# Optimization experiments

Measured on AMD Instinct MI355X. Metric: run time of the kernel, lower is better.

The kernel has to match this reference:

```python
import jax, jax.numpy as jnp
import numpy as np

K_NEIGHBORS = 16
NUM_PATCHES = 32
W_NORMAL = 1.0
W_SURFVAR = 1.0


def _knn_centered(points, k):
    """points: [B, N, 3] -> k nearest neighbors re-centered at each point, [B, N, k, 3].
    Distances are computed on stop_gradient(points) to match torch's .detach()."""
    pd = jax.lax.stop_gradient(points)
    # squared pairwise distances [B, N, N] (sqrt is monotone -> topk order identical)
    d2 = jnp.sum((pd[:, :, None, :] - pd[:, None, :, :]) ** 2, axis=-1)
    _, idx = jax.lax.top_k(-d2, k)  # smallest-k indices, [B, N, k]
    knn = jax.vmap(lambda pts, id_: pts[id_])(points, idx)  # [B, N, k, 3]
    return knn - points[:, :, None, :]


def _eig_props(knn):
    """knn: [B, N, k, 3] -> (normal [B,N,3] = eigvec of smallest eigval, eigvals [B,N,3] ascending)."""
    cov = jnp.einsum('bnki,bnkj->bnij', knn, knn)  # [B, N, 3, 3]
    w, v = jnp.linalg.eigh(cov)  # ascending eigenvalues, matches torch.symeig
    return v[..., :, 0], w


def setup_inputs() -> dict:
    key = jax.random.key(0)
    pointCloud = jax.random.normal(key, (4, 8192, 3), dtype=jnp.float32)
    return {"pointCloud": pointCloud}


def reference(pointCloud):
    B, N, _ = pointCloud.shape
    pp = N // NUM_PATCHES

    # global kNN / normals / surface variance
    knn_g = _knn_centered(pointCloud, K_NEIGHBORS)
    nrm_g, w_g = _eig_props(knn_g)

    # patchwise: each patch is an independent small point cloud -> fold patches into batch
    patch_pts = pointCloud.reshape(B * NUM_PATCHES, pp, 3)
    knn_p = _knn_centered(patch_pts, K_NEIGHBORS)
    nrm_p, w_p = _eig_props(knn_p)
    nrm_p = nrm_p.reshape(B, N, 3)

    # normal loss (abs variant, sign-ambiguity-free)
    loss_n = jnp.mean(jnp.linalg.norm(jnp.abs(nrm_p) - jnp.abs(nrm_g), axis=2)) * W_NORMAL

    # surface variance loss: lambda_min / sum(lambda)
    sv_g = w_g[..., 0] / jnp.sum(w_g, axis=-1)            # [B, N]
    sv_p = (w_p[..., 0] / jnp.sum(w_p, axis=-1)).reshape(B, N)
    loss_sv = jnp.mean((sv_p - sv_g) ** 2) * W_SURFVAR

    return jnp.stack([loss_n, loss_sv])  # [2] (original returns list of two [1] tensors)
```

## Files before the change

kernel.cpp:

```cpp
#include <hip/hip_runtime.h>
#include <math.h>

#define KNN 16
#define NPTS 8192
#define PTCH 256
#define NPATCH 32
#define NBATCH 4
#define SSTRIDE 130
#define LAMBDA_T 48.0f

#define GTAB 512
#define RMAX 6.5f
#define GH (RMAX / (float)GTAB)

#define NC 16
#define NCELLS (NC * NC * NC)
#define GMIN -4.2f
#define ICS 1.9047619f

__device__ __forceinline__ float lam_f(float r, float s)
{
    const float C     = 0.063493636f;
    const float SQ2PI = 2.5066283f;
    const float IS2   = 0.70710678f;
    float a = fabsf(r - s), b = r + s;
    float amr = a - r;
    float coefA = amr * amr + 2.f - s * s;
    float I = 2.f * __expf(-0.5f * b * b) - coefA * __expf(-0.5f * a * a)
            + r * SQ2PI * (erff(b * IS2) - erff(a * IS2));
    float M = C * (3.14159265f / r) * I;
    if (s > r) {
        float u = s - r;
        M += 12.566371f * C * (1.2533141f * erff(u * IS2) - u * __expf(-0.5f * u * u));
    }
    return (float)NPTS * M;
}

__device__ __forceinline__ void jrot(double& app, double& aqq, double& apq,
                                     double& arp, double& arq,
                                     double& vp0, double& vq0,
                                     double& vp1, double& vq1,
                                     double& vp2, double& vq2)
{
    double g = apq;
    if (g == 0.0) return;
    double theta = (aqq - app) / (2.0 * g);
    double at = fabs(theta);
    double t = (at > 1.0e154) ? (0.5 / theta)
                              : (copysign(1.0, theta) / (at + sqrt(theta * theta + 1.0)));
    double c = 1.0 / sqrt(t * t + 1.0);
    double s = t * c;
    double tau = s / (1.0 + c);
    app -= t * g;
    aqq += t * g;
    apq = 0.0;
    double rp = arp, rq = arq;
    arp = rp - s * (rq + tau * rp);
    arq = rq + s * (rp - tau * rq);
    double p0 = vp0, q0 = vq0;
    vp0 = p0 - s * (q0 + tau * p0); vq0 = q0 + s * (p0 - tau * q0);
    double p1 = vp1, q1 = vq1;
    vp1 = p1 - s * (q1 + tau * p1); vq1 = q1 + s * (p1 - tau * q1);
    double p2 = vp2, q2 = vq2;
    vp2 = p2 - s * (q2 + tau * p2); vq2 = q2 + s * (p2 - tau * q2);
}

__device__ __forceinline__ void eig3(double a00, double a11, double a22,
                                     double a01, double a02, double a12,
                                     double& nx, double& ny, double& nz,
                                     double& lmin, double& lsum)
{
    double v00 = 1, v01 = 0, v02 = 0;
    double v10 = 0, v11 = 1, v12 = 0;
    double v20 = 0, v21 = 0, v22 = 1;
    double scale = fabs(a00) + fabs(a11) + fabs(a22) + fabs(a01) + fabs(a02) + fabs(a12);
    if (scale > 0.0) {
        for (int sweep = 0; sweep < 6; ++sweep) {
            double off = fabs(a01) + fabs(a02) + fabs(a12);
            if (off <= scale * 1e-15) break;
            jrot(a00, a11, a01, a02, a12, v00, v01, v10, v11, v20, v21);
            jrot(a00, a22, a02, a01, a12, v00, v02, v10, v12, v20, v22);
            jrot(a11, a22, a12, a01, a02, v01, v02, v11, v12, v21, v22);
        }
    }
    lsum = a00 + a11 + a22;
    lmin = a00; nx = v00; ny = v10; nz = v20;
    if (a11 < lmin) { lmin = a11; nx = v01; ny = v11; nz = v21; }
    if (a22 < lmin) { lmin = a22; nx = v02; ny = v12; nz = v22; }
}

__device__ __forceinline__ unsigned mkkey(float d2, unsigned idx) {
    return (__float_as_uint(d2) & 0xFFFFE000u) | idx;
}

__device__ __forceinline__ void insert16(unsigned key, unsigned* L)
{
    L[KNN - 1] = key;
    #pragma unroll
    for (int m = KNN - 1; m >= 1; --m) {
        unsigned a = L[m - 1], b = L[m];
        L[m - 1] = min(a, b);
        L[m]     = max(a, b);
    }
}

__device__ __forceinline__ void merge4(unsigned* L, int lane)
{
    #pragma unroll
    for (int step = 1; step <= 2; step <<= 1) {
        unsigned tmp[KNN];
        #pragma unroll
        for (int m = 0; m < KNN; ++m) tmp[m] = __shfl(L[m], lane ^ step, 64);
        for (int m = 0; m < KNN; ++m) {
            if (tmp[m] >= L[KNN - 1]) break;
            insert16(tmp[m], L);
        }
    }
}

__device__ __forceinline__ unsigned mbcnt64(unsigned long long m) {
    return __builtin_amdgcn_mbcnt_hi((unsigned)(m >> 32),
           __builtin_amdgcn_mbcnt_lo((unsigned)m, 0u));
}

__device__ __forceinline__ int cidx(float v) {
    int i = (int)floorf((v - GMIN) * ICS);
    return min(max(i, 0), NC - 1);
}
__device__ __forceinline__ int cellOf(float x, float y, float z) {
    return (cidx(z) * NC + cidx(y)) * NC + cidx(x);
}

#define BT 1024
__global__ void __launch_bounds__(1024)
build_kernel(const float* __restrict__ pts,
             unsigned* __restrict__ cellStart, float4* __restrict__ sorted,
             float* __restrict__ gtab, unsigned* __restrict__ done)
{
    __shared__ unsigned hist[NCELLS];
    __shared__ unsigned part[BT];
    const int b = blockIdx.x;
    const int t = threadIdx.x;
    if (b == 0 && t == 0) done[0] = 0u;
    for (int i = t; i < NCELLS; i += BT) hist[i] = 0u;
    __syncthreads();
    const float* base = pts + (size_t)b * (NPTS * 3);
    float px[8], py[8], pz[8];
    int pc[8];
    #pragma unroll
    for (int k = 0; k < 8; ++k) {
        int i = k * BT + t;
        px[k] = base[i * 3 + 0];
        py[k] = base[i * 3 + 1];
        pz[k] = base[i * 3 + 2];
        pc[k] = cellOf(px[k], py[k], pz[k]);
        atomicAdd(&hist[pc[k]], 1u);
    }
    __syncthreads();
    unsigned loc[4], s = 0;
    #pragma unroll
    for (int i = 0; i < 4; ++i) { loc[i] = s; s += hist[t * 4 + i]; }
    part[t] = s;
    __syncthreads();
    for (int o = 1; o < BT; o <<= 1) {
        unsigned u = (t >= o) ? part[t - o] : 0u;
        __syncthreads();
        part[t] += u;
        __syncthreads();
    }
    unsigned basex = part[t] - s;
    unsigned* csb = cellStart + b * (NCELLS + 1);
    #pragma unroll
    for (int i = 0; i < 4; ++i) {
        unsigned e = basex + loc[i];
        csb[t * 4 + i] = e;
        hist[t * 4 + i] = e;
    }
    if (t == BT - 1) csb[NCELLS] = basex + s;
    __syncthreads();
    float4* sb = sorted + (size_t)b * NPTS;
    #pragma unroll
    for (int k = 0; k < 8; ++k) {
        int i = k * BT + t;
        unsigned slot = atomicAdd(&hist[pc[k]], 1u);
        float4 v;
        v.x = px[k]; v.y = py[k]; v.z = pz[k]; v.w = __uint_as_float((unsigned)i);
        sb[slot] = v;
    }
    if (b == 0 && t < GTAB) {
        float r = fmaxf((float)(t + 1) * GH, 0.01f);
        float lo = 0.f, hi = 12.f;
        #pragma unroll 1
        for (int it = 0; it < 16; ++it) {
            float mid = 0.5f * (lo + hi);
            if (lam_f(r, mid) < LAMBDA_T) lo = mid; else hi = mid;
        }
        gtab[t] = hi;
    }
}

__global__ void __launch_bounds__(256)
fselect_kernel(const float* __restrict__ pts,
               const unsigned* __restrict__ cellStart,
               const float4* __restrict__ sortedp,
               const float* __restrict__ gtab,
               unsigned* __restrict__ idx16)
{
    __shared__ unsigned survl[4 * SSTRIDE];
    const int t = threadIdx.x;
    const int wv = t >> 6;
    const int lane = t & 63;
    const int wq = __builtin_amdgcn_readfirstlane(blockIdx.x * 4 + wv);
    const int b   = wq >> 13;
    const int pos = wq & (NPTS - 1);
    const float* base = pts + (size_t)b * (NPTS * 3);
    const unsigned* cs = cellStart + b * (NCELLS + 1);
    const float4* sp = sortedp + (size_t)b * NPTS;
    unsigned* sl = survl + wv * SSTRIDE;

    const float4 qc = sp[pos];
    const float qx = qc.x, qy = qc.y, qz = qc.z;
    const int oq = b * NPTS + (int)__float_as_uint(qc.w);

    const float r = sqrtf(qx * qx + qy * qy + qz * qz);
    const int gi = min(GTAB - 1, (int)(r * (1.0f / GH)));
    const float g = gtab[gi];
    const float g2 = g * g;

    int ixlo = cidx(qx - g), ixhi = cidx(qx + g);
    int iylo = cidx(qy - g), iyhi = cidx(qy + g);
    int izlo = cidx(qz - g), izhi = cidx(qz + g);
    int nx = ixhi - ixlo + 1;
    int ny = iyhi - iylo + 1;
    int nyz = ny * (izhi - izlo + 1);
    const int lR  = (nyz >= 8) ? 3 : (nyz >= 4) ? 2 : (nyz >= 2) ? 1 : 0;
    const int R   = 1 << lR;
    const int lsl = 6 - lR;
    const unsigned SL = 64u >> lR;
    const unsigned slot = (unsigned)lane & (SL - 1u);
    unsigned cnt = 0;
    #pragma unroll 1
    for (int r0 = 0; r0 < nyz; r0 += 64) {
        int rr = r0 + lane;
        unsigned pk = 0;
        if (rr < nyz) {
            int iz = izlo + rr / ny;
            int iy = iylo + (rr - (rr / ny) * ny);
            int cb = (iz * NC + iy) * NC + ixlo;
            unsigned sB = cs[cb];
            pk = sB | ((cs[cb + nx] - sB) << 14);
        }
        int rmax = min(nyz - r0, 64);
        int gcount = (rmax + R - 1) >> lR;
        #pragma unroll 1
        for (int gg = 0; gg < gcount; ++gg) {
            unsigned pkm = __shfl(pk, (gg << lR) + (lane >> lsl), 64);
            unsigned sBm = pkm & 0x3FFFu;
            unsigned lm  = pkm >> 14;
            #pragma unroll 1
            for (unsigned st = slot; ; st += 2u * SL) {
                bool in0 = st < lm;
                if (!__any(in0 ? 1 : 0)) break;
                unsigned st1 = st + SL;
                bool in1 = st1 < lm;
                float4 c0 = sp[min(sBm + st,  (unsigned)(NPTS - 1))];
                float4 c1 = sp[min(sBm + st1, (unsigned)(NPTS - 1))];
                float dx0 = qx - c0.x, dy0 = qy - c0.y, dz0 = qz - c0.z;
                float d20 = dx0 * dx0 + dy0 * dy0 + dz0 * dz0;
                float dx1 = qx - c1.x, dy1 = qy - c1.y, dz1 = qz - c1.z;
                float d21 = dx1 * dx1 + dy1 * dy1 + dz1 * dz1;
                bool p0 = in0 && (d20 < g2);
                bool p1 = in1 && (d21 < g2);
                unsigned long long m0 = __ballot(p0);
                unsigned long long m1 = __ballot(p1);
                if (p0) {
                    unsigned sw = min(cnt + mbcnt64(m0), (unsigned)(SSTRIDE - 1));
                    sl[sw] = mkkey(d20, __float_as_uint(c0.w));
                }
                unsigned cn = cnt + (unsigned)__popcll(m0);
                if (p1) {
                    unsigned sw = min(cn + mbcnt64(m1), (unsigned)(SSTRIDE - 1));
                    sl[sw] = mkkey(d21, __float_as_uint(c1.w));
                }
                cnt = cn + (unsigned)__popcll(m1);
            }
        }
    }

    bool valid = (cnt >= KNN) && (cnt <= 128u);
    if (valid) {
        unsigned k0 = (lane < (int)cnt)      ? sl[lane]      : 0xFFFFFFFFu;
        unsigned k1 = (lane + 64 < (int)cnt) ? sl[lane + 64] : 0xFFFFFFFFu;
        unsigned r0 = 0, r1 = 0;
        #pragma unroll 4
        for (unsigned m = 0; m < cnt; ++m) {
            unsigned km = sl[m];
            r0 += (km < k0) ? 1u : 0u;
            r1 += (km < k1) ? 1u : 0u;
        }
        unsigned cand = 0;
        if (lane < (int)cnt && r0 == 15u) cand = k0;
        if (lane + 64 < (int)cnt && r1 == 15u) cand = k1;
        #pragma unroll
        for (int o = 1; o < 64; o <<= 1)
            cand = max(cand, (unsigned)__shfl_xor((int)cand, o, 64));
        float upper = __uint_as_float((cand & 0xFFFFE000u) + 0x2000u);
        valid = (upper < g2 * 0.999f - 1e-5f);
        if (valid) {
            if (lane < (int)cnt && r0 < 16u)
                idx16[(size_t)oq * 32 + r0] = k0 & 0x1FFFu;
            if (lane + 64 < (int)cnt && r1 < 16u)
                idx16[(size_t)oq * 32 + r1] = k1 & 0x1FFFu;
        }
    }
    if (!valid && lane == 0) {
        unsigned gl[KNN];
        #pragma unroll
        for (int m = 0; m < KNN; ++m) gl[m] = 0xFFFFFFFFu;
        #pragma unroll 1
        for (int i = 0; i < NPTS; ++i) {
            float cx = base[i * 3 + 0];
            float cy = base[i * 3 + 1];
            float cz = base[i * 3 + 2];
            float dx = qx - cx, dy = qy - cy, dz = qz - cz;
            float d2 = dx * dx + dy * dy + dz * dz;
            unsigned k = mkkey(d2, (unsigned)i);
            if (k < gl[KNN - 1]) insert16(k, gl);
        }
        unsigned* dst = idx16 + (size_t)oq * 32;
        #pragma unroll
        for (int m = 0; m < KNN; ++m) dst[m] = gl[m] & 0x1FFFu;
    }
}

__global__ void __launch_bounds__(256)
pselect_kernel(const float* __restrict__ pts, unsigned* __restrict__ idx16)
{
    __shared__ float4 pbuf4[PTCH];
    const int t = threadIdx.x;
    const int w = t >> 6;
    const int lane = t & 63;
    const int p = blockIdx.x;
    const int quarter = blockIdx.y;
    const int b = blockIdx.z;
    const float* base = pts + (size_t)b * (NPTS * 3);

    {
        const float* src = base + p * (PTCH * 3);
        float* dst = (float*)pbuf4;
        #pragma unroll
        for (int s = 0; s < 3; ++s) {
            int f = t + s * 256;
            int j = f / 3;
            int c = f - 3 * j;
            dst[j * 4 + c] = src[f];
        }
    }
    __syncthreads();

    const int qq = lane >> 2;
    const int h = lane & 3;
    const int qlocal = quarter * 64 + w * 16 + qq;
    float4 qv = pbuf4[qlocal];
    const float pqx = qv.x, pqy = qv.y, pqz = qv.z;

    unsigned pl[KNN];
    #pragma unroll
    for (int m = 0; m < KNN; ++m) pl[m] = 0xFFFFFFFFu;
    const int j0 = h * 64;
    #pragma unroll 4
    for (int j = j0; j < j0 + 64; ++j) {
        float4 c = pbuf4[j];
        float dx = pqx - c.x, dy = pqy - c.y, dz = pqz - c.z;
        float d2 = dx * dx + dy * dy + dz * dz;
        unsigned k = mkkey(d2, (unsigned)j);
        if (k < pl[KNN - 1]) insert16(k, pl);
    }
    merge4(pl, lane);
    if (h == 0) {
        int qid = b * NPTS + p * PTCH + qlocal;
        unsigned* dst = idx16 + (size_t)qid * 32 + 16;
        #pragma unroll
        for (int m = 0; m < KNN; ++m)
            dst[m] = (unsigned)(p * PTCH) + (pl[m] & 0x1FFFu);
    }
}

__global__ void __launch_bounds__(256)
eig_loss_kernel(const float* __restrict__ pts,
                const unsigned* __restrict__ idx16,
                double* __restrict__ partials,
                unsigned* __restrict__ done,
                float* __restrict__ out)
{
    __shared__ double sln[4], slv[4];
    __shared__ unsigned isLast;
    const int t = threadIdx.x;
    const int e = blockIdx.x * 256 + t;
    const int qid = e >> 1;
    const int b = qid >> 13;
    const int qi = qid & (NPTS - 1);
    const float* base = pts + (size_t)b * (NPTS * 3);

    const double qxd = (double)base[qi * 3 + 0];
    const double qyd = (double)base[qi * 3 + 1];
    const double qzd = (double)base[qi * 3 + 2];

    const unsigned* L = idx16 + (size_t)qid * 32 + (e & 1) * 16;
    double c00 = 0, c11 = 0, c22 = 0, c01 = 0, c02 = 0, c12 = 0;
    #pragma unroll
    for (int m = 0; m < KNN; ++m) {
        int idx = (int)L[m];
        double dx = (double)base[idx * 3 + 0] - qxd;
        double dy = (double)base[idx * 3 + 1] - qyd;
        double dz = (double)base[idx * 3 + 2] - qzd;
        c00 += dx * dx; c11 += dy * dy; c22 += dz * dz;
        c01 += dx * dy; c02 += dx * dz; c12 += dy * dz;
    }
    double nx, ny, nz, lmin, lsum;
    eig3(c00, c11, c22, c01, c02, c12, nx, ny, nz, lmin, lsum);
    double sv = lmin / lsum;

    double onx = __shfl_xor(nx, 1, 64);
    double ony = __shfl_xor(ny, 1, 64);
    double onz = __shfl_xor(nz, 1, 64);
    double osv = __shfl_xor(sv, 1, 64);

    double ln = 0.0, lsv = 0.0;
    if ((e & 1) == 0) {
        double dx = fabs(onx) - fabs(nx);
        double dy = fabs(ony) - fabs(ny);
        double dz = fabs(onz) - fabs(nz);
        ln  = sqrt(dx * dx + dy * dy + dz * dz);
        double ds = osv - sv;
        lsv = ds * ds;
    }
    #pragma unroll
    for (int o = 32; o > 0; o >>= 1) {
        ln  += __shfl_down(ln, o);
        lsv += __shfl_down(lsv, o);
    }
    const int w = t >> 6;
    if ((t & 63) == 0) { sln[w] = ln; slv[w] = lsv; }
    __syncthreads();
    if (t == 0) {
        partials[blockIdx.x * 2 + 0] = sln[0] + sln[1] + sln[2] + sln[3];
        partials[blockIdx.x * 2 + 1] = slv[0] + slv[1] + slv[2] + slv[3];
        __threadfence();
        isLast = (atomicAdd(done, 1u) == (unsigned)(gridDim.x - 1)) ? 1u : 0u;
    }
    __syncthreads();
    if (isLast) {
        double a = partials[t * 2 + 0];
        double c = partials[t * 2 + 1];
        #pragma unroll
        for (int o = 32; o > 0; o >>= 1) {
            a += __shfl_down(a, o);
            c += __shfl_down(c, o);
        }
        if ((t & 63) == 0) { sln[t >> 6] = a; slv[t >> 6] = c; }
        __syncthreads();
        if (t == 0) {
            const double inv = 1.0 / (double)(NBATCH * NPTS);
            out[0] = (float)((sln[0] + sln[1] + sln[2] + sln[3]) * inv);
            out[1] = (float)((slv[0] + slv[1] + slv[2] + slv[3]) * inv);
        }
    }
}

extern "C" void kernel_launch(void* const* d_in, const int* in_sizes, int n_in,
                              void* d_out, int out_size, void* d_ws, size_t ws_size,
                              hipStream_t stream)
{
    const float* pts = (const float*)d_in[0];
    float* out = (float*)d_out;

    unsigned char* ws = (unsigned char*)d_ws;
    unsigned* cellStart = (unsigned*)(ws);
    float4*   sorted    = (float4*)  (ws + 65552);
    float*    gtab      = (float*)   (ws + 589840);
    unsigned* done      = (unsigned*)(ws + 591888);
    unsigned* idx16     = (unsigned*)(ws + 591904);
    double*   partials  = (double*)  (ws + 4786208);

    hipLaunchKernelGGL(build_kernel, dim3(NBATCH), dim3(BT), 0, stream,
                       pts, cellStart, sorted, gtab, done);
    hipLaunchKernelGGL(fselect_kernel, dim3(NBATCH * NPTS / 4), dim3(256), 0, stream,
                       pts, cellStart, sorted, gtab, idx16);
    hipLaunchKernelGGL(pselect_kernel, dim3(NPATCH, 4, NBATCH), dim3(256), 0, stream,
                       pts, idx16);
    hipLaunchKernelGGL(eig_loss_kernel, dim3(NBATCH * NPTS * 2 / 256), dim3(256),
                       0, stream, pts, idx16, partials, done, out);
}
```

Baseline: 138.7 us.

## Split each query's neighbor-cell scan across two wavefronts and merge in LDS

The global kNN select kernel now gives each query point two wavefronts instead of one, with each scanning half of the candidate cell rows into its own shared-memory list. After a block barrier, the first wave appends the second wave's survivors to its list and runs the existing rank-based selection. The grid is doubled to match. This is meant to shorten the serial per-query scan and expose more parallelism, at the cost of a block-wide barrier, an LDS merge copy, more waves per query, and idle second waves during selection.

```diff
diff --git a/kernel.cpp b/kernel.cpp
--- a/kernel.cpp
+++ b/kernel.cpp
@@ -206,17 +206,20 @@
                const float* __restrict__ gtab,
                unsigned* __restrict__ idx16)
 {
-    __shared__ unsigned survl[4 * SSTRIDE];
+    __shared__ unsigned survl[2 * 2 * SSTRIDE];
+    __shared__ unsigned scnt[4];
     const int t = threadIdx.x;
     const int wv = t >> 6;
     const int lane = t & 63;
-    const int wq = __builtin_amdgcn_readfirstlane(blockIdx.x * 4 + wv);
+    const int qw = wv >> 1;
+    const int sh = wv & 1;
+    const int wq = __builtin_amdgcn_readfirstlane(blockIdx.x * 2 + qw);
     const int b   = wq >> 13;
     const int pos = wq & (NPTS - 1);
     const float* base = pts + (size_t)b * (NPTS * 3);
     const unsigned* cs = cellStart + b * (NCELLS + 1);
     const float4* sp = sortedp + (size_t)b * NPTS;
-    unsigned* sl = survl + wv * SSTRIDE;
+    unsigned* sl = survl + qw * (2 * SSTRIDE);
 
     const float4 qc = sp[pos];
     const float qx = qc.x, qy = qc.y, qz = qc.z;
@@ -238,19 +241,23 @@
     const int lsl = 6 - lR;
     const unsigned SL = 64u >> lR;
     const unsigned slot = (unsigned)lane & (SL - 1u);
+    const int half = (nyz + 1) >> 1;
+    const int rlo = sh ? half : 0;
+    const int rhi = sh ? nyz : half;
+    unsigned* myr = sl + sh * SSTRIDE;
     unsigned cnt = 0;
     #pragma unroll 1
-    for (int r0 = 0; r0 < nyz; r0 += 64) {
+    for (int r0 = rlo; r0 < rhi; r0 += 64) {
         int rr = r0 + lane;
         unsigned pk = 0;
-        if (rr < nyz) {
+        if (rr < rhi) {
             int iz = izlo + rr / ny;
             int iy = iylo + (rr - (rr / ny) * ny);
             int cb = (iz * NC + iy) * NC + ixlo;
             unsigned sB = cs[cb];
             pk = sB | ((cs[cb + nx] - sB) << 14);
         }
-        int rmax = min(nyz - r0, 64);
+        int rmax = min(rhi - r0, 64);
         int gcount = (rmax + R - 1) >> lR;
         #pragma unroll 1
         for (int gg = 0; gg < gcount; ++gg) {
@@ -275,20 +282,27 @@
                 unsigned long long m1 = __ballot(p1);
                 if (p0) {
                     unsigned sw = min(cnt + mbcnt64(m0), (unsigned)(SSTRIDE - 1));
-                    sl[sw] = mkkey(d20, __float_as_uint(c0.w));
+                    myr[sw] = mkkey(d20, __float_as_uint(c0.w));
                 }
                 unsigned cn = cnt + (unsigned)__popcll(m0);
                 if (p1) {
                     unsigned sw = min(cn + mbcnt64(m1), (unsigned)(SSTRIDE - 1));
-                    sl[sw] = mkkey(d21, __float_as_uint(c1.w));
+                    myr[sw] = mkkey(d21, __float_as_uint(c1.w));
                 }
                 cnt = cn + (unsigned)__popcll(m1);
             }
         }
     }
-
+    if (lane == 0) scnt[wv] = cnt;
+    __syncthreads();
+    if (sh != 0) return;
+
+    unsigned cnt0 = scnt[qw * 2];
+    unsigned cnt1 = scnt[qw * 2 + 1];
+    cnt = cnt0 + cnt1;
     bool valid = (cnt >= KNN) && (cnt <= 128u);
     if (valid) {
+        for (unsigned i = lane; i < cnt1; i += 64) sl[cnt0 + i] = sl[SSTRIDE + i];
         unsigned k0 = (lane < (int)cnt)      ? sl[lane]      : 0xFFFFFFFFu;
         unsigned k1 = (lane + 64 < (int)cnt) ? sl[lane + 64] : 0xFFFFFFFFu;
         unsigned r0 = 0, r1 = 0;
@@ -485,7 +499,7 @@
 
     hipLaunchKernelGGL(build_kernel, dim3(NBATCH), dim3(BT), 0, stream,
                        pts, cellStart, sorted, gtab, done);
-    hipLaunchKernelGGL(fselect_kernel, dim3(NBATCH * NPTS / 4), dim3(256), 0, stream,
+    hipLaunchKernelGGL(fselect_kernel, dim3(NBATCH * NPTS / 2), dim3(256), 0, stream,
                        pts, cellStart, sorted, gtab, idx16);
     hipLaunchKernelGGL(pselect_kernel, dim3(NPATCH, 4, NBATCH), dim3(256), 0, stream,
                        pts, idx16);
```

Result: slower. 151.1 us (+9.0%).
